# Kernel optimization log

Hardware: AMD Instinct MI355X
Metric: run time of the kernel (lower is better)

## Reference

```python
import jax, jax.numpy as jnp
import numpy as np

N_NODES = 50000
N_EDGES = 800000
IN_DIM = 96
OUT_DIM = 96
EDGE_DIM = 32
BN_EPS = 1e-5


def setup_inputs() -> dict:
    key = jax.random.key(0)
    ks = jax.random.split(key, 12)
    x = jax.random.normal(ks[0], (N_NODES, IN_DIM), dtype=jnp.float32)
    edge_index = jax.random.randint(ks[1], (2, N_EDGES), 0, N_NODES, dtype=jnp.int64)
    edge_attr = jax.random.normal(ks[2], (N_EDGES, EDGE_DIM), dtype=jnp.float32)
    # GINEConv edge projection Linear(edge_dim, in_dim)
    We = jax.random.normal(ks[3], (EDGE_DIM, IN_DIM), dtype=jnp.float32) / np.sqrt(EDGE_DIM)
    be = jnp.zeros((IN_DIM,), dtype=jnp.float32)
    # MLP: Linear(in_dim, out_dim) -> ReLU -> Linear(out_dim, out_dim)
    W1 = jax.random.normal(ks[4], (IN_DIM, OUT_DIM), dtype=jnp.float32) / np.sqrt(IN_DIM)
    b1 = jnp.zeros((OUT_DIM,), dtype=jnp.float32)
    W2 = jax.random.normal(ks[5], (OUT_DIM, OUT_DIM), dtype=jnp.float32) / np.sqrt(OUT_DIM)
    b2 = jnp.zeros((OUT_DIM,), dtype=jnp.float32)
    # BatchNorm1d affine params
    gamma = jnp.ones((OUT_DIM,), dtype=jnp.float32)
    beta = jnp.zeros((OUT_DIM,), dtype=jnp.float32)
    return {"x": x, "edge_index": edge_index, "edge_attr": edge_attr,
            "We": We, "be": be, "W1": W1, "b1": b1, "W2": W2, "b2": b2,
            "gamma": gamma, "beta": beta}


def reference(x, edge_index, edge_attr, We, be, W1, b1, W2, b2, gamma, beta):
    src = edge_index[0]  # x_j (message source)
    dst = edge_index[1]  # aggregation target
    # GINE message: ReLU(x_j + Lin(edge_attr)) per edge  [E, in_dim]
    msg = jax.nn.relu(x[src] + edge_attr @ We + be)
    # sum aggregation into dst nodes  [N, in_dim]
    aggr = jax.ops.segment_sum(msg, dst, num_segments=x.shape[0])
    # (1 + eps) * x + aggr, eps = 0 (GINEConv default)
    h = x + aggr
    # MLP: Linear -> ReLU -> Linear
    h = jax.nn.relu(h @ W1 + b1) @ W2 + b2
    # BatchNorm1d (training-mode batch statistics) + affine
    mean = jnp.mean(h, axis=0)
    var = jnp.mean(jnp.square(h - mean), axis=0)  # biased var, as torch BN uses
    h = (h - mean) * jax.lax.rsqrt(var + BN_EPS) * gamma + beta
    # ReLU (dropout is identity in eval / deterministic reference)
    return jax.nn.relu(h)
```

## Files before the change

### kernel.cpp

```cpp
#include <hip/hip_runtime.h>

typedef unsigned short ushort_t;
typedef unsigned int uint_t;
typedef __attribute__((ext_vector_type(8))) short bf16x8;
typedef __attribute__((ext_vector_type(4))) float f32x4;
typedef __attribute__((ext_vector_type(2))) float f32x2;

#define N_NODES 50000
#define N_EDGES 800000
#define BN_EPS 1e-5f

#define OFF_STATS 4800000
#define OFF_FLAG  4800192

#define SC_PAIR    0
#define SC_OFFSETS 1600000
#define SC_DEG     1650016
#define SC_RANK    1700032
#define SC_BSUM    2500032
#define SC_BBASE   2500288

#define NB_SCAN 196

__device__ __forceinline__ ushort_t f2bf(float f) {
    uint_t u = __float_as_uint(f);
    uint_t r = ((u >> 16) & 1u) + 0x7fffu;
    return (ushort_t)((u + r) >> 16);
}

__global__ __launch_bounds__(1024) void detect_kernel(const int* __restrict__ ei,
                                                      int* __restrict__ flag) {
    __shared__ int any_nonzero;
    if (threadIdx.x == 0) any_nonzero = 0;
    __syncthreads();
    int nz = 0;
#pragma unroll
    for (int q = 0; q < 4; ++q) {
        int p = 1 + 2 * (threadIdx.x * 4 + q) * 195;
        if (ei[p] != 0) nz = 1;
    }
    if (nz) atomicOr(&any_nonzero, 1);
    __syncthreads();
    if (threadIdx.x == 0) *flag = any_nonzero ? 0 : 1;
}

__global__ __launch_bounds__(256) void hist_kernel(const int* __restrict__ ei,
                                                   const int* __restrict__ flag,
                                                   int* __restrict__ deg,
                                                   int* __restrict__ rank) {
    const int is64 = *flag;
    const int stride = gridDim.x * blockDim.x;
    for (int e = blockIdx.x * blockDim.x + threadIdx.x; e < N_EDGES; e += stride) {
        int s, d;
        if (is64) { s = ei[2 * e]; d = ei[2 * N_EDGES + 2 * e]; }
        else      { s = ei[e];     d = ei[N_EDGES + e]; }
        if ((uint_t)s < N_NODES && (uint_t)d < N_NODES)
            rank[e] = atomicAdd(&deg[d], 1);
    }
}

__global__ __launch_bounds__(256) void scan1_kernel(const int* __restrict__ deg,
                                                    int* __restrict__ bsum) {
    __shared__ int sd[256];
    const int t = threadIdx.x;
    const int i = blockIdx.x * 256 + t;
    sd[t] = (i < N_NODES) ? deg[i] : 0;
    __syncthreads();
    for (int s = 128; s > 0; s >>= 1) {
        if (t < s) sd[t] += sd[t + s];
        __syncthreads();
    }
    if (t == 0) bsum[blockIdx.x] = sd[0];
}

__global__ __launch_bounds__(256) void scan2_kernel(const int* __restrict__ bsum,
                                                    int* __restrict__ bbase) {
    __shared__ int sd[256];
    const int t = threadIdx.x;
    int v = (t < NB_SCAN) ? bsum[t] : 0;
    sd[t] = v;
    __syncthreads();
    for (int off = 1; off < 256; off <<= 1) {
        int u = (t >= off) ? sd[t - off] : 0;
        __syncthreads();
        sd[t] += u;
        __syncthreads();
    }
    if (t < NB_SCAN) bbase[t] = sd[t] - v;
}

__global__ __launch_bounds__(256) void scan3_kernel(const int* __restrict__ deg,
                                                    const int* __restrict__ bbase,
                                                    int* __restrict__ offsets) {
    __shared__ int sd[256];
    const int t = threadIdx.x;
    const int i = blockIdx.x * 256 + t;
    const int v = (i < N_NODES) ? deg[i] : 0;
    sd[t] = v;
    __syncthreads();
    for (int off = 1; off < 256; off <<= 1) {
        int u = (t >= off) ? sd[t - off] : 0;
        __syncthreads();
        sd[t] += u;
        __syncthreads();
    }
    const int excl = bbase[blockIdx.x] + sd[t] - v;
    if (i < N_NODES) offsets[i] = excl;
    if (i == N_NODES - 1) offsets[N_NODES] = excl + v;
}

__global__ __launch_bounds__(256) void scatter_kernel(const int* __restrict__ ei,
                                                      const int* __restrict__ flag,
                                                      const int* __restrict__ offsets,
                                                      const int* __restrict__ rank,
                                                      int2* __restrict__ pair) {
    const int is64 = *flag;
    const int stride = gridDim.x * blockDim.x;
    for (int e = blockIdx.x * blockDim.x + threadIdx.x; e < N_EDGES; e += stride) {
        int s, d;
        if (is64) { s = ei[2 * e]; d = ei[2 * N_EDGES + 2 * e]; }
        else      { s = ei[e];     d = ei[N_EDGES + e]; }
        if ((uint_t)s < N_NODES && (uint_t)d < N_NODES) {
            const int pos = offsets[d] + rank[e];
            pair[pos] = make_int2(e, s);
        }
    }
}

__global__ __launch_bounds__(256) void node_aggr_kernel(
    const float* __restrict__ x, const float* __restrict__ ea,
    const float* __restrict__ We, const float* __restrict__ be,
    const int2* __restrict__ pair, const int* __restrict__ offsets,
    float* __restrict__ hbuf) {
    const int lane = threadIdx.x & 63;
    const int q = lane >> 4;
    const int t = lane & 15;
    const int wav = blockIdx.x * (blockDim.x >> 6) + (threadIdx.x >> 6);
    const int nwav = gridDim.x * (blockDim.x >> 6);

    bf16x8 Bf[6];
    float ben[6];
#pragma unroll
    for (int f = 0; f < 6; ++f) {
        const int n = t + 16 * f;
#pragma unroll
        for (int j = 0; j < 8; ++j) {
            const int k = q * 8 + j;
            Bf[f][j] = (short)f2bf(We[k * 96 + n]);
        }
        ben[f] = be[n];
    }

    for (int n = wav; n < N_NODES; n += nwav) {
        const int off = offsets[n];
        const int deg = offsets[n + 1] - off;

        float part[6];
#pragma unroll
        for (int f = 0; f < 6; ++f) part[f] = 0.f;

        for (int c0 = 0; c0 < deg; c0 += 16) {
            const int rem = deg - c0;
            int eid_t = -1, src_t = -1;
            if (t < rem) {
                const int2 p = pair[off + c0 + t];
                eid_t = p.x;
                src_t = p.y;
            }
            bf16x8 A = {0, 0, 0, 0, 0, 0, 0, 0};
            if (eid_t >= 0) {
                const float* row = ea + (size_t)eid_t * 32 + q * 8;
                f32x4 a0 = *(const f32x4*)(row);
                f32x4 a1 = *(const f32x4*)(row + 4);
#pragma unroll
                for (int j = 0; j < 4; ++j) {
                    A[j] = (short)f2bf(a0[j]);
                    A[4 + j] = (short)f2bf(a1[j]);
                }
            }

            f32x4 acc[6];
#pragma unroll
            for (int f = 0; f < 6; ++f) {
                f32x4 z = {0.f, 0.f, 0.f, 0.f};
                acc[f] = __builtin_amdgcn_mfma_f32_16x16x32_bf16(A, Bf[f], z, 0, 0, 0);
            }

            int s_r[4];
#pragma unroll
            for (int r = 0; r < 4; ++r) s_r[r] = __shfl(src_t, q * 4 + r);

#pragma unroll
            for (int r = 0; r < 4; ++r) {
                const int m = q * 4 + r;
                if (m < rem) {
                    const float* xrow = x + (size_t)s_r[r] * 96;
#pragma unroll
                    for (int f = 0; f < 6; ++f) {
                        float v = acc[f][r] + ben[f] + xrow[t + 16 * f];
                        part[f] += v > 0.f ? v : 0.f;
                    }
                }
            }
        }

#pragma unroll
        for (int f = 0; f < 6; ++f) {
            part[f] += __shfl_xor(part[f], 16);
            part[f] += __shfl_xor(part[f], 32);
        }

        if (q == 0) {
            const float* xn = x + (size_t)n * 96;
            float* hn = hbuf + (size_t)n * 96;
#pragma unroll
            for (int f = 0; f < 6; ++f) {
                const int col = t + 16 * f;
                hn[col] = part[f] + xn[col];
            }
        }
    }
}

#define MTILE 64
__global__ __launch_bounds__(256) void mlp_kernel(
    float* buf, const float* __restrict__ W1g, const float* __restrict__ b1g,
    const float* __restrict__ W2g, const float* __restrict__ b2g,
    float* __restrict__ stats) {
    __shared__ float Ws[96 * 96];
    __shared__ float hsT[96][68];

    const int tid = threadIdx.x;
    const int fg = tid & 15;
    const int ng = tid >> 4;
    const int n0 = blockIdx.x * MTILE;

    for (int i = tid; i < 96 * 96 / 4; i += 256)
        ((f32x4*)Ws)[i] = ((const f32x4*)W1g)[i];
    for (int i = tid; i < MTILE * 96 / 4; i += 256) {
        const int base = i * 4;
        const int nn = base / 96, k = base - nn * 96;
        f32x4 v = {0.f, 0.f, 0.f, 0.f};
        if (n0 + nn < N_NODES)
            v = *(const f32x4*)(buf + (size_t)(n0 + nn) * 96 + k);
        hsT[k][nn] = v[0]; hsT[k + 1][nn] = v[1];
        hsT[k + 2][nn] = v[2]; hsT[k + 3][nn] = v[3];
    }
    __syncthreads();

    float acc[4][6];
#pragma unroll
    for (int ff = 0; ff < 6; ++ff) {
        const float b = b1g[6 * fg + ff];
        acc[0][ff] = b; acc[1][ff] = b; acc[2][ff] = b; acc[3][ff] = b;
    }
    for (int k = 0; k < 96; ++k) {
        const f32x4 a = *(const f32x4*)&hsT[k][4 * ng];
        const float* wr = &Ws[k * 96 + 6 * fg];
        const f32x2 w01 = *(const f32x2*)(wr);
        const f32x2 w23 = *(const f32x2*)(wr + 2);
        const f32x2 w45 = *(const f32x2*)(wr + 4);
        const float w[6] = {w01[0], w01[1], w23[0], w23[1], w45[0], w45[1]};
#pragma unroll
        for (int nn = 0; nn < 4; ++nn)
#pragma unroll
            for (int ff = 0; ff < 6; ++ff) acc[nn][ff] += a[nn] * w[ff];
    }
    __syncthreads();

#pragma unroll
    for (int nn = 0; nn < 4; ++nn)
#pragma unroll
        for (int ff = 0; ff < 6; ++ff) {
            float v = acc[nn][ff];
            hsT[6 * fg + ff][4 * ng + nn] = v > 0.f ? v : 0.f;
        }
    for (int i = tid; i < 96 * 96 / 4; i += 256)
        ((f32x4*)Ws)[i] = ((const f32x4*)W2g)[i];
    __syncthreads();

#pragma unroll
    for (int ff = 0; ff < 6; ++ff) {
        const float b = b2g[6 * fg + ff];
        acc[0][ff] = b; acc[1][ff] = b; acc[2][ff] = b; acc[3][ff] = b;
    }
    for (int k = 0; k < 96; ++k) {
        const f32x4 a = *(const f32x4*)&hsT[k][4 * ng];
        const float* wr = &Ws[k * 96 + 6 * fg];
        const f32x2 w01 = *(const f32x2*)(wr);
        const f32x2 w23 = *(const f32x2*)(wr + 2);
        const f32x2 w45 = *(const f32x2*)(wr + 4);
        const float w[6] = {w01[0], w01[1], w23[0], w23[1], w45[0], w45[1]};
#pragma unroll
        for (int nn = 0; nn < 4; ++nn)
#pragma unroll
            for (int ff = 0; ff < 6; ++ff) acc[nn][ff] += a[nn] * w[ff];
    }

#pragma unroll
    for (int nn = 0; nn < 4; ++nn) {
        const int n = n0 + 4 * ng + nn;
        if (n < N_NODES) {
            float* o = buf + (size_t)n * 96 + 6 * fg;
            *(f32x2*)(o)     = (f32x2){acc[nn][0], acc[nn][1]};
            *(f32x2*)(o + 2) = (f32x2){acc[nn][2], acc[nn][3]};
            *(f32x2*)(o + 4) = (f32x2){acc[nn][4], acc[nn][5]};
        }
    }

    __syncthreads();
#pragma unroll
    for (int nn = 0; nn < 4; ++nn)
#pragma unroll
        for (int ff = 0; ff < 6; ++ff)
            hsT[6 * fg + ff][4 * ng + nn] = acc[nn][ff];
    __syncthreads();

    if (tid < 96) {
        int nmax = N_NODES - n0;
        if (nmax > MTILE) nmax = MTILE;
        float s = 0.f, s2 = 0.f;
        for (int n = 0; n < nmax; ++n) {
            const float v = hsT[tid][n];
            s += v; s2 += v * v;
        }
        atomicAdd(&stats[tid], s);
        atomicAdd(&stats[96 + tid], s2);
    }
}

__global__ __launch_bounds__(256) void bn_kernel(
    const float* __restrict__ h2, const float* __restrict__ stats,
    const float* __restrict__ gamma, const float* __restrict__ beta,
    float* __restrict__ out) {
    __shared__ float sc[96], sh[96];
    const int tid = threadIdx.x;
    if (tid < 96) {
        const float inv_n = 1.f / (float)N_NODES;
        const float mean = stats[tid] * inv_n;
        float var = stats[96 + tid] * inv_n - mean * mean;
        var = var > 0.f ? var : 0.f;
        const float s = gamma[tid] * rsqrtf(var + BN_EPS);
        sc[tid] = s;
        sh[tid] = beta[tid] - mean * s;
    }
    __syncthreads();
    const int total4 = N_NODES * 96 / 4;
    for (int i = blockIdx.x * blockDim.x + tid; i < total4;
         i += gridDim.x * blockDim.x) {
        f32x4 v = ((const f32x4*)h2)[i];
        const int jb = (i * 4) % 96;
#pragma unroll
        for (int c = 0; c < 4; ++c) {
            float u = v[c] * sc[jb + c] + sh[jb + c];
            v[c] = u > 0.f ? u : 0.f;
        }
        ((f32x4*)out)[i] = v;
    }
}

extern "C" void kernel_launch(void* const* d_in, const int* in_sizes, int n_in,
                              void* d_out, int out_size, void* d_ws,
                              size_t ws_size, hipStream_t stream) {
    const float* x     = (const float*)d_in[0];
    const int*   ei    = (const int*)d_in[1];
    const float* ea    = (const float*)d_in[2];
    const float* We    = (const float*)d_in[3];
    const float* be    = (const float*)d_in[4];
    const float* W1    = (const float*)d_in[5];
    const float* b1    = (const float*)d_in[6];
    const float* W2    = (const float*)d_in[7];
    const float* b2    = (const float*)d_in[8];
    const float* gamma = (const float*)d_in[9];
    const float* beta  = (const float*)d_in[10];
    float* out = (float*)d_out;

    float* ws    = (float*)d_ws;
    float* hbuf  = ws;
    float* stats = ws + OFF_STATS;
    int*   flag  = (int*)(ws + OFF_FLAG);

    int*  scratch = (int*)d_out;
    int2* pair    = (int2*)(scratch + SC_PAIR);
    int*  offsets = scratch + SC_OFFSETS;
    int*  deg     = scratch + SC_DEG;
    int*  rank    = scratch + SC_RANK;
    int*  bsum    = scratch + SC_BSUM;
    int*  bbase   = scratch + SC_BBASE;

    hipMemsetAsync((void*)stats, 0, 256 * sizeof(float), stream);
    hipMemsetAsync((void*)deg, 0, N_NODES * sizeof(int), stream);

    detect_kernel<<<1, 1024, 0, stream>>>(ei, flag);
    hist_kernel<<<1024, 256, 0, stream>>>(ei, flag, deg, rank);
    scan1_kernel<<<NB_SCAN, 256, 0, stream>>>(deg, bsum);
    scan2_kernel<<<1, 256, 0, stream>>>(bsum, bbase);
    scan3_kernel<<<NB_SCAN, 256, 0, stream>>>(deg, bbase, offsets);
    scatter_kernel<<<1024, 256, 0, stream>>>(ei, flag, offsets, rank, pair);
    node_aggr_kernel<<<2048, 256, 0, stream>>>(x, ea, We, be, pair, offsets,
                                               hbuf);
    mlp_kernel<<<(N_NODES + MTILE - 1) / MTILE, 256, 0, stream>>>(
        hbuf, W1, b1, W2, b2, stats);
    bn_kernel<<<1024, 256, 0, stream>>>(hbuf, stats, gamma, beta, out);
}
```

Before: 392.8 us.

## Fuse graph preprocessing and MLP/BN stages into cooperative persistent kernels

Replaces the chain of nine small launches plus memsets with two cooperative kernels. Stages are separated by grid.sync: detect, histogram, a two-pass scan, scatter and aggregation in one kernel, and MLP tiles followed by BN in the other. The scan is reworked from three passes to two. The aim is to remove per-launch overhead and the host-side memsets. In exchange, grid-wide barriers are added and the grid is capped by occupancy, which may cut parallelism in the aggregation and MLP phases; a non-cooperative fallback remains if the launch fails.

```diff
diff --git a/kernel.cpp b/kernel.cpp
--- a/kernel.cpp
+++ b/kernel.cpp
@@ -1,4 +1,7 @@
 #include <hip/hip_runtime.h>
+#include <hip/hip_cooperative_groups.h>
+
+namespace cg = cooperative_groups;
 
 typedef unsigned short ushort_t;
 typedef unsigned int uint_t;
@@ -18,9 +21,10 @@
 #define SC_DEG     1650016
 #define SC_RANK    1700032
 #define SC_BSUM    2500032
-#define SC_BBASE   2500288
 
 #define NB_SCAN 196
+#define MTILE 64
+#define NTILES ((N_NODES + MTILE - 1) / MTILE)
 
 __device__ __forceinline__ ushort_t f2bf(float f) {
     uint_t u = __float_as_uint(f);
@@ -28,29 +32,12 @@
     return (ushort_t)((u + r) >> 16);
 }
 
-__global__ __launch_bounds__(1024) void detect_kernel(const int* __restrict__ ei,
-                                                      int* __restrict__ flag) {
-    __shared__ int any_nonzero;
-    if (threadIdx.x == 0) any_nonzero = 0;
-    __syncthreads();
-    int nz = 0;
-#pragma unroll
-    for (int q = 0; q < 4; ++q) {
-        int p = 1 + 2 * (threadIdx.x * 4 + q) * 195;
-        if (ei[p] != 0) nz = 1;
-    }
-    if (nz) atomicOr(&any_nonzero, 1);
-    __syncthreads();
-    if (threadIdx.x == 0) *flag = any_nonzero ? 0 : 1;
-}
-
-__global__ __launch_bounds__(256) void hist_kernel(const int* __restrict__ ei,
-                                                   const int* __restrict__ flag,
-                                                   int* __restrict__ deg,
-                                                   int* __restrict__ rank) {
-    const int is64 = *flag;
-    const int stride = gridDim.x * blockDim.x;
-    for (int e = blockIdx.x * blockDim.x + threadIdx.x; e < N_EDGES; e += stride) {
+
+__device__ __forceinline__ void dev_hist(const int* __restrict__ ei, int is64,
+                                         int* __restrict__ deg,
+                                         int* __restrict__ rank,
+                                         int gtid, int nth) {
+    for (int e = gtid; e < N_EDGES; e += nth) {
         int s, d;
         if (is64) { s = ei[2 * e]; d = ei[2 * N_EDGES + 2 * e]; }
         else      { s = ei[e];     d = ei[N_EDGES + e]; }
@@ -59,84 +46,64 @@
     }
 }
 
-__global__ __launch_bounds__(256) void scan1_kernel(const int* __restrict__ deg,
-                                                    int* __restrict__ bsum) {
-    __shared__ int sd[256];
-    const int t = threadIdx.x;
-    const int i = blockIdx.x * 256 + t;
-    sd[t] = (i < N_NODES) ? deg[i] : 0;
-    __syncthreads();
-    for (int s = 128; s > 0; s >>= 1) {
-        if (t < s) sd[t] += sd[t + s];
-        __syncthreads();
-    }
-    if (t == 0) bsum[blockIdx.x] = sd[0];
-}
-
-__global__ __launch_bounds__(256) void scan2_kernel(const int* __restrict__ bsum,
-                                                    int* __restrict__ bbase) {
-    __shared__ int sd[256];
-    const int t = threadIdx.x;
-    int v = (t < NB_SCAN) ? bsum[t] : 0;
-    sd[t] = v;
+__device__ __forceinline__ void dev_scanA(const int* __restrict__ deg,
+                                          int* __restrict__ offsets,
+                                          int* __restrict__ bsum,
+                                          int bid, int tid, int* sd) {
+    const int i = bid * 256 + tid;
+    const int v = (i < N_NODES) ? deg[i] : 0;
+    sd[tid] = v;
     __syncthreads();
     for (int off = 1; off < 256; off <<= 1) {
-        int u = (t >= off) ? sd[t - off] : 0;
-        __syncthreads();
-        sd[t] += u;
-        __syncthreads();
-    }
-    if (t < NB_SCAN) bbase[t] = sd[t] - v;
-}
-
-__global__ __launch_bounds__(256) void scan3_kernel(const int* __restrict__ deg,
-                                                    const int* __restrict__ bbase,
-                                                    int* __restrict__ offsets) {
-    __shared__ int sd[256];
-    const int t = threadIdx.x;
-    const int i = blockIdx.x * 256 + t;
-    const int v = (i < N_NODES) ? deg[i] : 0;
-    sd[t] = v;
+        int u = (tid >= off) ? sd[tid - off] : 0;
+        __syncthreads();
+        sd[tid] += u;
+        __syncthreads();
+    }
+    if (i < N_NODES) offsets[i] = sd[tid] - v;
+    if (tid == 255) bsum[bid] = sd[255];
+}
+
+__device__ __forceinline__ void dev_scanB(int* __restrict__ offsets,
+                                          const int* __restrict__ bsum,
+                                          int bid, int tid, int* sd) {
+    const int v = (tid < NB_SCAN) ? bsum[tid] : 0;
+    sd[tid] = v;
     __syncthreads();
     for (int off = 1; off < 256; off <<= 1) {
-        int u = (t >= off) ? sd[t - off] : 0;
-        __syncthreads();
-        sd[t] += u;
-        __syncthreads();
-    }
-    const int excl = bbase[blockIdx.x] + sd[t] - v;
-    if (i < N_NODES) offsets[i] = excl;
-    if (i == N_NODES - 1) offsets[N_NODES] = excl + v;
-}
-
-__global__ __launch_bounds__(256) void scatter_kernel(const int* __restrict__ ei,
-                                                      const int* __restrict__ flag,
-                                                      const int* __restrict__ offsets,
-                                                      const int* __restrict__ rank,
-                                                      int2* __restrict__ pair) {
-    const int is64 = *flag;
-    const int stride = gridDim.x * blockDim.x;
-    for (int e = blockIdx.x * blockDim.x + threadIdx.x; e < N_EDGES; e += stride) {
+        int u = (tid >= off) ? sd[tid - off] : 0;
+        __syncthreads();
+        sd[tid] += u;
+        __syncthreads();
+    }
+    const int base = (bid == 0) ? 0 : sd[bid - 1];
+    const int i = bid * 256 + tid;
+    if (i < N_NODES) offsets[i] += base;
+    if (bid == 0 && tid == 0) offsets[N_NODES] = sd[NB_SCAN - 1];
+}
+
+__device__ __forceinline__ void dev_scatter(const int* __restrict__ ei, int is64,
+                                            const int* __restrict__ offsets,
+                                            const int* __restrict__ rank,
+                                            int2* __restrict__ pair,
+                                            int gtid, int nth) {
+    for (int e = gtid; e < N_EDGES; e += nth) {
         int s, d;
         if (is64) { s = ei[2 * e]; d = ei[2 * N_EDGES + 2 * e]; }
         else      { s = ei[e];     d = ei[N_EDGES + e]; }
-        if ((uint_t)s < N_NODES && (uint_t)d < N_NODES) {
-            const int pos = offsets[d] + rank[e];
-            pair[pos] = make_int2(e, s);
-        }
-    }
-}
-
-__global__ __launch_bounds__(256) void node_aggr_kernel(
+        if ((uint_t)s < N_NODES && (uint_t)d < N_NODES)
+            pair[offsets[d] + rank[e]] = make_int2(e, s);
+    }
+}
+
+__device__ __forceinline__ void dev_node_aggr(
     const float* __restrict__ x, const float* __restrict__ ea,
     const float* __restrict__ We, const float* __restrict__ be,
     const int2* __restrict__ pair, const int* __restrict__ offsets,
-    float* __restrict__ hbuf) {
+    float* __restrict__ hbuf, int wav, int nwav) {
     const int lane = threadIdx.x & 63;
     const int q = lane >> 4;
     const int t = lane & 15;
-    const int wav = blockIdx.x * (blockDim.x >> 6) + (threadIdx.x >> 6);
-    const int nwav = gridDim.x * (blockDim.x >> 6);
 
     bf16x8 Bf[6];
     float ben[6];
@@ -222,18 +189,13 @@
     }
 }
 
-#define MTILE 64
-__global__ __launch_bounds__(256) void mlp_kernel(
+__device__ __forceinline__ void dev_mlp_tile(
     float* buf, const float* __restrict__ W1g, const float* __restrict__ b1g,
     const float* __restrict__ W2g, const float* __restrict__ b2g,
-    float* __restrict__ stats) {
-    __shared__ float Ws[96 * 96];
-    __shared__ float hsT[96][68];
-
+    float* __restrict__ stats, int n0, float* Ws, float (*hsT)[68]) {
     const int tid = threadIdx.x;
     const int fg = tid & 15;
     const int ng = tid >> 4;
-    const int n0 = blockIdx.x * MTILE;
 
     for (int i = tid; i < 96 * 96 / 4; i += 256)
         ((f32x4*)Ws)[i] = ((const f32x4*)W1g)[i];
@@ -329,11 +291,13 @@
     }
 }
 
-__global__ __launch_bounds__(256) void bn_kernel(
-    const float* __restrict__ h2, const float* __restrict__ stats,
-    const float* __restrict__ gamma, const float* __restrict__ beta,
-    float* __restrict__ out) {
-    __shared__ float sc[96], sh[96];
+__device__ __forceinline__ void dev_bn(const float* __restrict__ h2,
+                                       const float* __restrict__ stats,
+                                       const float* __restrict__ gamma,
+                                       const float* __restrict__ beta,
+                                       float* __restrict__ out,
+                                       float* sc, float* sh,
+                                       int gtid, int gstride) {
     const int tid = threadIdx.x;
     if (tid < 96) {
         const float inv_n = 1.f / (float)N_NODES;
@@ -346,8 +310,7 @@
     }
     __syncthreads();
     const int total4 = N_NODES * 96 / 4;
-    for (int i = blockIdx.x * blockDim.x + tid; i < total4;
-         i += gridDim.x * blockDim.x) {
+    for (int i = gtid; i < total4; i += gstride) {
         f32x4 v = ((const f32x4*)h2)[i];
         const int jb = (i * 4) % 96;
 #pragma unroll
@@ -357,6 +320,154 @@
         }
         ((f32x4*)out)[i] = v;
     }
+}
+
+
+__global__ __launch_bounds__(256, 4) void prep_aggr_kernel(
+    const float* __restrict__ x, const int* __restrict__ ei,
+    const float* __restrict__ ea, const float* __restrict__ We,
+    const float* __restrict__ be, float* __restrict__ hbuf,
+    float* __restrict__ stats, int* __restrict__ flag,
+    int* __restrict__ scratch) {
+    cg::grid_group grid = cg::this_grid();
+    __shared__ int sd[256];
+    __shared__ int s_any;
+
+    int2* pair   = (int2*)(scratch + SC_PAIR);
+    int* offsets = scratch + SC_OFFSETS;
+    int* deg     = scratch + SC_DEG;
+    int* rank    = scratch + SC_RANK;
+    int* bsum    = scratch + SC_BSUM;
+
+    const int tid = threadIdx.x;
+    const int bid = blockIdx.x;
+    const int nth = gridDim.x * 256;
+    const int gtid = bid * 256 + tid;
+
+    for (int i = gtid; i < N_NODES; i += nth) deg[i] = 0;
+    if (gtid < 256) stats[gtid] = 0.f;
+    if (bid == 0) {
+        if (tid == 0) s_any = 0;
+        __syncthreads();
+        int nz = 0;
+        for (int j = 0; j < 16; ++j) {
+            const int p = 1 + 2 * (tid * 16 + j) * 195;
+            if (ei[p] != 0) nz = 1;
+        }
+        if (nz) atomicOr(&s_any, 1);
+        __syncthreads();
+        if (tid == 0) *flag = s_any ? 0 : 1;
+    }
+    grid.sync();
+
+    const int is64 = *flag;
+    dev_hist(ei, is64, deg, rank, gtid, nth);
+    grid.sync();
+
+    if (bid < NB_SCAN) dev_scanA(deg, offsets, bsum, bid, tid, sd);
+    grid.sync();
+    if (bid < NB_SCAN) dev_scanB(offsets, bsum, bid, tid, sd);
+    grid.sync();
+
+    dev_scatter(ei, is64, offsets, rank, pair, gtid, nth);
+    grid.sync();
+
+    dev_node_aggr(x, ea, We, be, pair, offsets, hbuf,
+                  bid * 4 + (tid >> 6), gridDim.x * 4);
+}
+
+__global__ __launch_bounds__(256, 2) void mlp_bn_kernel(
+    float* buf, const float* __restrict__ W1g, const float* __restrict__ b1g,
+    const float* __restrict__ W2g, const float* __restrict__ b2g,
+    float* __restrict__ stats, const float* __restrict__ gamma,
+    const float* __restrict__ beta, float* __restrict__ out) {
+    cg::grid_group grid = cg::this_grid();
+    __shared__ float Ws[96 * 96];
+    __shared__ float hsT[96][68];
+    __shared__ float sc[96], sh[96];
+
+    for (int tile = blockIdx.x; tile < NTILES; tile += gridDim.x) {
+        dev_mlp_tile(buf, W1g, b1g, W2g, b2g, stats, tile * MTILE, Ws, hsT);
+        __syncthreads();
+    }
+    grid.sync();
+
+    dev_bn(buf, stats, gamma, beta, out, sc, sh,
+           blockIdx.x * 256 + threadIdx.x, gridDim.x * 256);
+}
+
+
+__global__ __launch_bounds__(1024) void detect_kernel(const int* __restrict__ ei,
+                                                      int* __restrict__ flag) {
+    __shared__ int any_nonzero;
+    if (threadIdx.x == 0) any_nonzero = 0;
+    __syncthreads();
+    int nz = 0;
+#pragma unroll
+    for (int q = 0; q < 4; ++q) {
+        int p = 1 + 2 * (threadIdx.x * 4 + q) * 195;
+        if (ei[p] != 0) nz = 1;
+    }
+    if (nz) atomicOr(&any_nonzero, 1);
+    __syncthreads();
+    if (threadIdx.x == 0) *flag = any_nonzero ? 0 : 1;
+}
+
+__global__ __launch_bounds__(256) void hist_kernel(const int* __restrict__ ei,
+                                                   const int* __restrict__ flag,
+                                                   int* __restrict__ deg,
+                                                   int* __restrict__ rank) {
+    dev_hist(ei, *flag, deg, rank, blockIdx.x * 256 + threadIdx.x,
+             gridDim.x * 256);
+}
+
+__global__ __launch_bounds__(256) void scanA_kernel(const int* __restrict__ deg,
+                                                    int* __restrict__ offsets,
+                                                    int* __restrict__ bsum) {
+    __shared__ int sd[256];
+    dev_scanA(deg, offsets, bsum, blockIdx.x, threadIdx.x, sd);
+}
+
+__global__ __launch_bounds__(256) void scanB_kernel(int* __restrict__ offsets,
+                                                    const int* __restrict__ bsum) {
+    __shared__ int sd[256];
+    dev_scanB(offsets, bsum, blockIdx.x, threadIdx.x, sd);
+}
+
+__global__ __launch_bounds__(256) void scatter_kernel(const int* __restrict__ ei,
+                                                      const int* __restrict__ flag,
+                                                      const int* __restrict__ offsets,
+                                                      const int* __restrict__ rank,
+                                                      int2* __restrict__ pair) {
+    dev_scatter(ei, *flag, offsets, rank, pair,
+                blockIdx.x * 256 + threadIdx.x, gridDim.x * 256);
+}
+
+__global__ __launch_bounds__(256) void node_aggr_kernel(
+    const float* __restrict__ x, const float* __restrict__ ea,
+    const float* __restrict__ We, const float* __restrict__ be,
+    const int2* __restrict__ pair, const int* __restrict__ offsets,
+    float* __restrict__ hbuf) {
+    dev_node_aggr(x, ea, We, be, pair, offsets, hbuf,
+                  blockIdx.x * 4 + (threadIdx.x >> 6), gridDim.x * 4);
+}
+
+__global__ __launch_bounds__(256) void mlp_kernel(
+    float* buf, const float* __restrict__ W1g, const float* __restrict__ b1g,
+    const float* __restrict__ W2g, const float* __restrict__ b2g,
+    float* __restrict__ stats) {
+    __shared__ float Ws[96 * 96];
+    __shared__ float hsT[96][68];
+    dev_mlp_tile(buf, W1g, b1g, W2g, b2g, stats, blockIdx.x * MTILE, Ws, hsT);
+}
+
+__global__ __launch_bounds__(256) void bn_kernel(
+    const float* __restrict__ h2, const float* __restrict__ stats,
+    const float* __restrict__ gamma, const float* __restrict__ beta,
+    float* __restrict__ out) {
+    __shared__ float sc[96], sh[96];
+    dev_bn(h2, stats, gamma, beta, out, sc, sh,
+           blockIdx.x * 256 + threadIdx.x, gridDim.x * 256);
 }
 
 extern "C" void kernel_launch(void* const* d_in, const int* in_sizes, int n_in,
@@ -378,7 +489,7 @@
     float* ws    = (float*)d_ws;
     float* hbuf  = ws;
     float* stats = ws + OFF_STATS;
-    int*   flag  = (int*)(ws + OFF_FLAG);
+    int*   flagp = (int*)(ws + OFF_FLAG);
 
     int*  scratch = (int*)d_out;
     int2* pair    = (int2*)(scratch + SC_PAIR);
@@ -386,20 +497,42 @@
     int*  deg     = scratch + SC_DEG;
     int*  rank    = scratch + SC_RANK;
     int*  bsum    = scratch + SC_BSUM;
-    int*  bbase   = scratch + SC_BBASE;
-
-    hipMemsetAsync((void*)stats, 0, 256 * sizeof(float), stream);
-    hipMemsetAsync((void*)deg, 0, N_NODES * sizeof(int), stream);
-
-    detect_kernel<<<1, 1024, 0, stream>>>(ei, flag);
-    hist_kernel<<<1024, 256, 0, stream>>>(ei, flag, deg, rank);
-    scan1_kernel<<<NB_SCAN, 256, 0, stream>>>(deg, bsum);
-    scan2_kernel<<<1, 256, 0, stream>>>(bsum, bbase);
-    scan3_kernel<<<NB_SCAN, 256, 0, stream>>>(deg, bbase, offsets);
-    scatter_kernel<<<1024, 256, 0, stream>>>(ei, flag, offsets, rank, pair);
-    node_aggr_kernel<<<2048, 256, 0, stream>>>(x, ea, We, be, pair, offsets,
-                                               hbuf);
-    mlp_kernel<<<(N_NODES + MTILE - 1) / MTILE, 256, 0, stream>>>(
-        hbuf, W1, b1, W2, b2, stats);
-    bn_kernel<<<1024, 256, 0, stream>>>(hbuf, stats, gamma, beta, out);
-}
+
+    static int g1 = 0, g2 = 0;
+    if (g1 == 0) {
+        int b1n = 0, b2n = 0;
+        if (hipOccupancyMaxActiveBlocksPerMultiprocessor(
+                &b1n, (const void*)prep_aggr_kernel, 256, 0) != hipSuccess ||
+            b1n < 1) b1n = 1;
+        if (hipOccupancyMaxActiveBlocksPerMultiprocessor(
+                &b2n, (const void*)mlp_bn_kernel, 256, 0) != hipSuccess ||
+            b2n < 1) b2n = 1;
+        g1 = b1n * 256 > 1024 ? 1024 : b1n * 256;
+        g2 = b2n * 256 > 512 ? 512 : b2n * 256;
+    }
+
+    void* a1[] = {(void*)&x, (void*)&ei, (void*)&ea, (void*)&We, (void*)&be,
+                  (void*)&hbuf, (void*)&stats, (void*)&flagp, (void*)&scratch};
+    hipError_t e1 = hipLaunchCooperativeKernel(
+        (const void*)prep_aggr_kernel, dim3(g1), dim3(256), a1, 0, stream);
+    if (e1 != hipSuccess) {
+        hipMemsetAsync((void*)stats, 0, 256 * sizeof(float), stream);
+        hipMemsetAsync((void*)deg, 0, N_NODES * sizeof(int), stream);
+        detect_kernel<<<1, 1024, 0, stream>>>(ei, flagp);
+        hist_kernel<<<1024, 256, 0, stream>>>(ei, flagp, deg, rank);
+        scanA_kernel<<<NB_SCAN, 256, 0, stream>>>(deg, offsets, bsum);
+        scanB_kernel<<<NB_SCAN, 256, 0, stream>>>(offsets, bsum);
+        scatter_kernel<<<1024, 256, 0, stream>>>(ei, flagp, offsets, rank, pair);
+        node_aggr_kernel<<<1024, 256, 0, stream>>>(x, ea, We, be, pair, offsets,
+                                                   hbuf);
+    }
+
+    void* a2[] = {(void*)&hbuf, (void*)&W1, (void*)&b1, (void*)&W2, (void*)&b2,
+                  (void*)&stats, (void*)&gamma, (void*)&beta, (void*)&out};
+    hipError_t e2 = hipLaunchCooperativeKernel(
+        (const void*)mlp_bn_kernel, dim3(g2), dim3(256), a2, 0, stream);
+    if (e2 != hipSuccess) {
+        mlp_kernel<<<NTILES, 256, 0, stream>>>(hbuf, W1, b1, W2, b2, stats);
+        bn_kernel<<<1024, 256, 0, stream>>>(hbuf, stats, gamma, beta, out);
+    }
+}
```

New measurement: 785.2 us. 2x slower.

## Fuse CSR scan stages and memsets to cut kernel launches

Applied to the files above, without the earlier changes.

Folds the two memsets and the edge-index dtype detection into one init kernel. It also merges the three-pass prefix scan into one local-scan kernel, and each consumer block rebuilds the block-sum prefix in shared memory. This removes several launches and the serial single-block scan between stages. In exchange, every scatter and aggregation block repeats a small 196-element scan and adds an extra indirection when computing offsets.

```diff
diff --git a/kernel.cpp b/kernel.cpp
--- a/kernel.cpp
+++ b/kernel.cpp
@@ -13,14 +13,15 @@
 #define OFF_STATS 4800000
 #define OFF_FLAG  4800192
 
-#define SC_PAIR    0
-#define SC_OFFSETS 1600000
-#define SC_DEG     1650016
-#define SC_RANK    1700032
-#define SC_BSUM    2500032
-#define SC_BBASE   2500288
+#define SC_PAIR  0
+#define SC_LEXCL 1600000
+#define SC_DEG   1650016
+#define SC_RANK  1700032
+#define SC_BSUM  2500032
 
 #define NB_SCAN 196
+#define MTILE 64
+#define NTILES ((N_NODES + MTILE - 1) / MTILE)
 
 __device__ __forceinline__ ushort_t f2bf(float f) {
     uint_t u = __float_as_uint(f);
@@ -28,20 +29,28 @@
     return (ushort_t)((u + r) >> 16);
 }
 
-__global__ __launch_bounds__(1024) void detect_kernel(const int* __restrict__ ei,
-                                                      int* __restrict__ flag) {
-    __shared__ int any_nonzero;
-    if (threadIdx.x == 0) any_nonzero = 0;
-    __syncthreads();
-    int nz = 0;
-#pragma unroll
-    for (int q = 0; q < 4; ++q) {
-        int p = 1 + 2 * (threadIdx.x * 4 + q) * 195;
-        if (ei[p] != 0) nz = 1;
-    }
-    if (nz) atomicOr(&any_nonzero, 1);
-    __syncthreads();
-    if (threadIdx.x == 0) *flag = any_nonzero ? 0 : 1;
+__global__ __launch_bounds__(256) void init_kernel(const int* __restrict__ ei,
+                                                   int* __restrict__ flag,
+                                                   int* __restrict__ deg,
+                                                   float* __restrict__ stats) {
+    const int gtid = blockIdx.x * 256 + threadIdx.x;
+    const int nth = gridDim.x * 256;
+    for (int i = gtid; i < N_NODES; i += nth) deg[i] = 0;
+    if (gtid < 256) stats[gtid] = 0.f;
+    if (blockIdx.x == 0) {
+        __shared__ int s_any;
+        if (threadIdx.x == 0) s_any = 0;
+        __syncthreads();
+        int nz = 0;
+#pragma unroll
+        for (int j = 0; j < 16; ++j) {
+            const int p = 1 + 2 * (threadIdx.x * 16 + j) * 195;
+            if (ei[p] != 0) nz = 1;
+        }
+        if (nz) atomicOr(&s_any, 1);
+        __syncthreads();
+        if (threadIdx.x == 0) *flag = s_any ? 0 : 1;
+    }
 }
 
 __global__ __launch_bounds__(256) void hist_kernel(const int* __restrict__ ei,
@@ -59,61 +68,53 @@
     }
 }
 
-__global__ __launch_bounds__(256) void scan1_kernel(const int* __restrict__ deg,
+__global__ __launch_bounds__(256) void scanA_kernel(const int* __restrict__ deg,
+                                                    int* __restrict__ lexcl,
                                                     int* __restrict__ bsum) {
     __shared__ int sd[256];
-    const int t = threadIdx.x;
-    const int i = blockIdx.x * 256 + t;
-    sd[t] = (i < N_NODES) ? deg[i] : 0;
-    __syncthreads();
-    for (int s = 128; s > 0; s >>= 1) {
-        if (t < s) sd[t] += sd[t + s];
-        __syncthreads();
-    }
-    if (t == 0) bsum[blockIdx.x] = sd[0];
-}
-
-__global__ __launch_bounds__(256) void scan2_kernel(const int* __restrict__ bsum,
-                                                    int* __restrict__ bbase) {
-    __shared__ int sd[256];
-    const int t = threadIdx.x;
-    int v = (t < NB_SCAN) ? bsum[t] : 0;
-    sd[t] = v;
+    const int tid = threadIdx.x;
+    const int i = blockIdx.x * 256 + tid;
+    const int v = (i < N_NODES) ? deg[i] : 0;
+    sd[tid] = v;
     __syncthreads();
     for (int off = 1; off < 256; off <<= 1) {
-        int u = (t >= off) ? sd[t - off] : 0;
-        __syncthreads();
-        sd[t] += u;
-        __syncthreads();
-    }
-    if (t < NB_SCAN) bbase[t] = sd[t] - v;
-}
-
-__global__ __launch_bounds__(256) void scan3_kernel(const int* __restrict__ deg,
-                                                    const int* __restrict__ bbase,
-                                                    int* __restrict__ offsets) {
-    __shared__ int sd[256];
-    const int t = threadIdx.x;
-    const int i = blockIdx.x * 256 + t;
-    const int v = (i < N_NODES) ? deg[i] : 0;
-    sd[t] = v;
+        int u = (tid >= off) ? sd[tid - off] : 0;
+        __syncthreads();
+        sd[tid] += u;
+        __syncthreads();
+    }
+    if (i < N_NODES) lexcl[i] = sd[tid] - v;
+    if (tid == 255) bsum[blockIdx.x] = sd[255];
+}
+
+__device__ __forceinline__ void build_sbase(const int* __restrict__ bsum,
+                                            int* sd, int* sbase, int* tot) {
+    const int tid = threadIdx.x;
+    const int v = (tid < NB_SCAN) ? bsum[tid] : 0;
+    sd[tid] = v;
     __syncthreads();
     for (int off = 1; off < 256; off <<= 1) {
-        int u = (t >= off) ? sd[t - off] : 0;
-        __syncthreads();
-        sd[t] += u;
-        __syncthreads();
-    }
-    const int excl = bbase[blockIdx.x] + sd[t] - v;
-    if (i < N_NODES) offsets[i] = excl;
-    if (i == N_NODES - 1) offsets[N_NODES] = excl + v;
+        int u = (tid >= off) ? sd[tid - off] : 0;
+        __syncthreads();
+        sd[tid] += u;
+        __syncthreads();
+    }
+    if (tid < NB_SCAN) sbase[tid] = sd[tid] - v;
+    if (tid == NB_SCAN - 1) *tot = sd[tid];
+    __syncthreads();
 }
 
 __global__ __launch_bounds__(256) void scatter_kernel(const int* __restrict__ ei,
                                                       const int* __restrict__ flag,
-                                                      const int* __restrict__ offsets,
+                                                      const int* __restrict__ lexcl,
+                                                      const int* __restrict__ bsum,
                                                       const int* __restrict__ rank,
                                                       int2* __restrict__ pair) {
+    __shared__ int sd[256];
+    __shared__ int sbase[NB_SCAN];
+    __shared__ int tot;
+    build_sbase(bsum, sd, sbase, &tot);
+
     const int is64 = *flag;
     const int stride = gridDim.x * blockDim.x;
     for (int e = blockIdx.x * blockDim.x + threadIdx.x; e < N_EDGES; e += stride) {
@@ -121,7 +122,7 @@
         if (is64) { s = ei[2 * e]; d = ei[2 * N_EDGES + 2 * e]; }
         else      { s = ei[e];     d = ei[N_EDGES + e]; }
         if ((uint_t)s < N_NODES && (uint_t)d < N_NODES) {
-            const int pos = offsets[d] + rank[e];
+            const int pos = sbase[d >> 8] + lexcl[d] + rank[e];
             pair[pos] = make_int2(e, s);
         }
     }
@@ -130,13 +131,18 @@
 __global__ __launch_bounds__(256) void node_aggr_kernel(
     const float* __restrict__ x, const float* __restrict__ ea,
     const float* __restrict__ We, const float* __restrict__ be,
-    const int2* __restrict__ pair, const int* __restrict__ offsets,
-    float* __restrict__ hbuf) {
+    const int2* __restrict__ pair, const int* __restrict__ lexcl,
+    const int* __restrict__ bsum, float* __restrict__ hbuf) {
+    __shared__ int sd[256];
+    __shared__ int sbase[NB_SCAN];
+    __shared__ int tot;
+    build_sbase(bsum, sd, sbase, &tot);
+
     const int lane = threadIdx.x & 63;
     const int q = lane >> 4;
     const int t = lane & 15;
-    const int wav = blockIdx.x * (blockDim.x >> 6) + (threadIdx.x >> 6);
-    const int nwav = gridDim.x * (blockDim.x >> 6);
+    const int wav = blockIdx.x * 4 + (threadIdx.x >> 6);
+    const int nwav = gridDim.x * 4;
 
     bf16x8 Bf[6];
     float ben[6];
@@ -152,8 +158,10 @@
     }
 
     for (int n = wav; n < N_NODES; n += nwav) {
-        const int off = offsets[n];
-        const int deg = offsets[n + 1] - off;
+        const int off = sbase[n >> 8] + lexcl[n];
+        const int offn = (n + 1 == N_NODES) ? tot
+                         : sbase[(n + 1) >> 8] + lexcl[n + 1];
+        const int deg = offn - off;
 
         float part[6];
 #pragma unroll
@@ -222,7 +230,6 @@
     }
 }
 
-#define MTILE 64
 __global__ __launch_bounds__(256) void mlp_kernel(
     float* buf, const float* __restrict__ W1g, const float* __restrict__ b1g,
     const float* __restrict__ W2g, const float* __restrict__ b2g,
@@ -378,28 +385,21 @@
     float* ws    = (float*)d_ws;
     float* hbuf  = ws;
     float* stats = ws + OFF_STATS;
-    int*   flag  = (int*)(ws + OFF_FLAG);
+    int*   flagp = (int*)(ws + OFF_FLAG);
 
     int*  scratch = (int*)d_out;
     int2* pair    = (int2*)(scratch + SC_PAIR);
-    int*  offsets = scratch + SC_OFFSETS;
+    int*  lexcl   = scratch + SC_LEXCL;
     int*  deg     = scratch + SC_DEG;
     int*  rank    = scratch + SC_RANK;
     int*  bsum    = scratch + SC_BSUM;
-    int*  bbase   = scratch + SC_BBASE;
-
-    hipMemsetAsync((void*)stats, 0, 256 * sizeof(float), stream);
-    hipMemsetAsync((void*)deg, 0, N_NODES * sizeof(int), stream);
-
-    detect_kernel<<<1, 1024, 0, stream>>>(ei, flag);
-    hist_kernel<<<1024, 256, 0, stream>>>(ei, flag, deg, rank);
-    scan1_kernel<<<NB_SCAN, 256, 0, stream>>>(deg, bsum);
-    scan2_kernel<<<1, 256, 0, stream>>>(bsum, bbase);
-    scan3_kernel<<<NB_SCAN, 256, 0, stream>>>(deg, bbase, offsets);
-    scatter_kernel<<<1024, 256, 0, stream>>>(ei, flag, offsets, rank, pair);
-    node_aggr_kernel<<<2048, 256, 0, stream>>>(x, ea, We, be, pair, offsets,
-                                               hbuf);
-    mlp_kernel<<<(N_NODES + MTILE - 1) / MTILE, 256, 0, stream>>>(
-        hbuf, W1, b1, W2, b2, stats);
+
+    init_kernel<<<NB_SCAN, 256, 0, stream>>>(ei, flagp, deg, stats);
+    hist_kernel<<<1024, 256, 0, stream>>>(ei, flagp, deg, rank);
+    scanA_kernel<<<NB_SCAN, 256, 0, stream>>>(deg, lexcl, bsum);
+    scatter_kernel<<<1024, 256, 0, stream>>>(ei, flagp, lexcl, bsum, rank, pair);
+    node_aggr_kernel<<<2048, 256, 0, stream>>>(x, ea, We, be, pair, lexcl,
+                                               bsum, hbuf);
+    mlp_kernel<<<NTILES, 256, 0, stream>>>(hbuf, W1, b1, W2, b2, stats);
     bn_kernel<<<1024, 256, 0, stream>>>(hbuf, stats, gamma, beta, out);
 }
```

Result: no change. 390.0 us (-0.7%).
